# Performance work log

Hardware: AMD Instinct MI355X
Metric: run time of the kernel (lower is better)

## Reference

```python
import jax, jax.numpy as jnp
import numpy as np

DIM = 1024; HEADS = 16; HEAD = 64; FFN_H = 4096
LE = 8; TOPK = 2; DIM_E = 512; DIM_S = 1024
B = 1; S = 2048; N = B * S; NMOE = 2
THETA = 10000.0; EPS = 1e-6; RSF = 1.0


def rmsnorm(x, g):
    return x * jax.lax.rsqrt(jnp.mean(x * x, axis=-1, keepdims=True) + EPS) * g


def rotary(x):
    # x: [b, h, s, a]; matches RotaryEmb: split halves, y1=x1*cos+x2*sin, y2=-x1*sin+x2*cos
    a = x.shape[-1]; s = x.shape[2]
    inv_freq = (1.0 / THETA) ** (jnp.arange(0, a, 2, dtype=jnp.float32) / a)
    freqs = jnp.arange(s, dtype=jnp.float32)[:, None] * inv_freq[None, :]  # [s, a/2]
    cos, sin = jnp.cos(freqs), jnp.sin(freqs)
    x1, x2 = jnp.split(x, 2, axis=-1)
    return jnp.concatenate([x1 * cos + x2 * sin, -x1 * sin + x2 * cos], axis=-1)


def attention(x, attn_w, attn_o, doc):
    # causal + same-document masked attention (flex_attention mask_mod equivalent)
    b, s, d = x.shape
    xq, xk, xv = jnp.split(x @ attn_w, 3, axis=-1)
    def heads(t):
        return t.reshape(b, s, HEADS, HEAD).transpose(0, 2, 1, 3)
    xq, xk, xv = heads(xq), heads(xk), heads(xv)
    xq, xk = rotary(xq), rotary(xk)
    scores = jnp.einsum('bhqa,bhka->bhqk', xq, xk) / jnp.sqrt(jnp.float32(HEAD))
    q_idx = jnp.arange(s)
    mask = (q_idx[:, None] >= q_idx[None, :])[None] & (doc[:, :, None] == doc[:, None, :])
    scores = jnp.where(mask[:, None, :, :], scores, -jnp.inf)
    probs = jax.nn.softmax(scores, axis=-1)
    out = jnp.einsum('bhqk,bhka->bhqa', probs, xv)
    return out.transpose(0, 2, 1, 3).reshape(b, s, d) @ attn_o


def dense_layer(x, aw, ao, up, down, ag, fg, doc):
    xi = attention(rmsnorm(x, ag), aw, ao, doc) + x
    xf = rmsnorm(xi, fg)
    x1, x2 = jnp.split(xf @ up, 2, axis=-1)
    return (jax.nn.silu(x1) * x2) @ down + xi


def moe_layer(x, aw, ao, ag, fg, experts, tkeys, rbias, sup, sdown, idx, vals, doc):
    xi = attention(rmsnorm(x, ag), aw, ao, doc) + x
    xf = rmsnorm(xi, fg)                     # [b,s,d]
    flat = xf.reshape(-1, DIM)               # [N,d]
    # routing: base values + token-key logits + bias, sigmoid, renormalize
    tv = flat @ tkeys                        # [N,le]
    vals = vals + jnp.take_along_axis(tv, idx, axis=-1) + rbias[idx]
    sc = jax.nn.sigmoid(vals)
    sc = sc / jnp.sum(sc, axis=-1, keepdims=True) * RSF   # [N,k]
    # grouped-gemm experts (SwiGLU per expert); dense-over-experts then gather
    h1 = jnp.einsum('nd,edh->neh', flat, experts[0])
    h2 = jnp.einsum('nd,edh->neh', flat, experts[1])
    y_all = jnp.einsum('neh,edh->ned', jax.nn.silu(h1) * h2, experts[2])
    y_sel = jnp.take_along_axis(y_all, idx[:, :, None], axis=1)   # [N,k,d]
    y = jnp.sum(y_sel * sc[:, :, None], axis=1).reshape(xf.shape)
    # shared expert
    x1, x2 = jnp.split(xf @ sup, 2, axis=-1)
    y = y + (jax.nn.silu(x1) * x2) @ sdown
    return y + xi


def setup_inputs() -> dict:
    key = jax.random.key(0)
    ks = jax.random.split(key, 24)
    w = lambda k, shp: (jax.random.normal(k, shp, dtype=jnp.float32) * 0.02)
    inp = {
        'x': jax.random.normal(ks[0], (B, S, DIM), dtype=jnp.float32),
        'doc': jnp.sort(jax.random.randint(ks[1], (B, S), 0, 4), axis=-1).astype(jnp.int32),
        'indices': jax.random.randint(ks[2], (NMOE, N, TOPK), 0, LE).astype(jnp.int64),
        'values': jax.random.normal(ks[3], (NMOE, N, TOPK), dtype=jnp.float32),
        # 2 dense layers (first_k=1, last_k=1)
        'dense_attn_w': w(ks[4], (2, DIM, 3 * DIM)),
        'dense_attn_o': w(ks[5], (2, DIM, DIM)),
        'dense_ffn_up': w(ks[6], (2, DIM, 2 * FFN_H)),
        'dense_ffn_down': w(ks[7], (2, FFN_H, DIM)),
        'dense_attn_g': jnp.ones((2, DIM), dtype=jnp.float32),
        'dense_ffn_g': jnp.ones((2, DIM), dtype=jnp.float32),
        # 2 MoE layers
        'moe_attn_w': w(ks[8], (NMOE, DIM, 3 * DIM)),
        'moe_attn_o': w(ks[9], (NMOE, DIM, DIM)),
        'moe_attn_g': jnp.ones((NMOE, DIM), dtype=jnp.float32),
        'moe_ffn_g': jnp.ones((NMOE, DIM), dtype=jnp.float32),
        'moe_experts': w(ks[10], (NMOE, 3, LE, DIM, DIM_E)),
        'moe_token_keys': w(ks[11], (NMOE, DIM, LE)),
        'moe_router_bias': jnp.zeros((NMOE, LE), dtype=jnp.float32),
        'moe_shared_up': w(ks[12], (NMOE, DIM, 2 * DIM_S)),
        'moe_shared_down': w(ks[13], (NMOE, DIM_S, DIM)),
    }
    return inp


def reference(x, doc, indices, values, dense_attn_w, dense_attn_o, dense_ffn_up,
              dense_ffn_down, dense_attn_g, dense_ffn_g, moe_attn_w, moe_attn_o,
              moe_attn_g, moe_ffn_g, moe_experts, moe_token_keys, moe_router_bias,
              moe_shared_up, moe_shared_down):
    x = dense_layer(x, dense_attn_w[0], dense_attn_o[0], dense_ffn_up[0],
                    dense_ffn_down[0], dense_attn_g[0], dense_ffn_g[0], doc)
    for i in range(NMOE):
        x = moe_layer(x, moe_attn_w[i], moe_attn_o[i], moe_attn_g[i], moe_ffn_g[i],
                      moe_experts[i], moe_token_keys[i], moe_router_bias[i],
                      moe_shared_up[i], moe_shared_down[i], indices[i], values[i], doc)
    x = dense_layer(x, dense_attn_w[1], dense_attn_o[1], dense_ffn_up[1],
                    dense_ffn_down[1], dense_attn_g[1], dense_ffn_g[1], doc)
    return x
```

## Files before the change

### kernel.cpp

```cpp
#include <hip/hip_runtime.h>
#include <cmath>
#include <cstddef>
#include <cstdint>

#define DIMM   1024
#define HEADS  16
#define HEADD  64
#define FFN_H  4096
#define LE     8
#define TOPK   2
#define DIM_E  512
#define DIM_S  1024
#define NTOK   2048

typedef __bf16 bf16x8 __attribute__((ext_vector_type(8)));
typedef float  f32x4  __attribute__((ext_vector_type(4)));

union BF4 { __bf16 h[4]; uint2 u; };
union BF2 { __bf16 h[2]; uint32_t u; };

__device__ __forceinline__ void ldg_lds16(const __bf16* g, __bf16* l) {
    __builtin_amdgcn_global_load_lds(
        (const __attribute__((address_space(1))) uint32_t*)g,
        (__attribute__((address_space(3))) uint32_t*)l, 16, 0, 0);
}

__global__ __launch_bounds__(256) void rmsnorm_bf(
    const float* __restrict__ x, const float* __restrict__ g,
    __bf16* __restrict__ y)
{
    const int row = blockIdx.x;
    const int t = threadIdx.x;
    const float* xr = x + (size_t)row * DIMM;
    float4 v = *(const float4*)(xr + t * 4);
    float ss = v.x * v.x + v.y * v.y + v.z * v.z + v.w * v.w;
    #pragma unroll
    for (int off = 32; off > 0; off >>= 1) ss += __shfl_down(ss, off, 64);
    __shared__ float ws[4];
    if ((t & 63) == 0) ws[t >> 6] = ss;
    __syncthreads();
    const float tot = ws[0] + ws[1] + ws[2] + ws[3];
    const float scale = rsqrtf(tot * (1.0f / DIMM) + 1e-6f);
    const float4 gv = *(const float4*)(g + t * 4);
    BF4 o;
    o.h[0] = (__bf16)(v.x * scale * gv.x);
    o.h[1] = (__bf16)(v.y * scale * gv.y);
    o.h[2] = (__bf16)(v.z * scale * gv.z);
    o.h[3] = (__bf16)(v.w * scale * gv.w);
    *(uint2*)(y + (size_t)row * DIMM + t * 4) = o.u;
}

template <typename OutT>
__global__ __launch_bounds__(256) void gemm_bf_t(
    const __bf16* __restrict__ A, const __bf16* __restrict__ BT,
    const float* __restrict__ add, OutT* __restrict__ C,
    int M, int N, int K)
{
    __shared__ __bf16 As[128 * 32];
    __shared__ __bf16 Bs[128 * 32];
    const int t = threadIdx.x;
    const int m0 = blockIdx.y * 128, n0 = blockIdx.x * 128;
    const int lane = t & 63;
    const int wv = t >> 6;
    const int mw = (wv >> 1) * 64, nw = (wv & 1) * 64;
    const int fr = lane & 15;
    const int fk = ((lane >> 4) ^ ((fr >> 1) & 3)) * 8;
    const int r0 = t >> 2;
    const int q0l = (t & 3) * 8;
    const int q0s = ((t & 3) ^ ((t >> 3) & 3)) * 8;

    const __bf16* gA0 = A + (size_t)(m0 + r0) * K + q0s;
    const __bf16* gA1 = A + (size_t)(m0 + 64 + r0) * K + q0s;
    const __bf16* gB0 = BT + (size_t)(n0 + r0) * K + q0s;
    const __bf16* gB1 = BT + (size_t)(n0 + 64 + r0) * K + q0s;
    __bf16* lA0 = &As[r0 * 32 + q0l];
    __bf16* lA1 = &As[(64 + r0) * 32 + q0l];
    __bf16* lB0 = &Bs[r0 * 32 + q0l];
    __bf16* lB1 = &Bs[(64 + r0) * 32 + q0l];

    f32x4 acc[4][4];
    #pragma unroll
    for (int i = 0; i < 4; ++i)
        #pragma unroll
        for (int j = 0; j < 4; ++j) acc[i][j] = (f32x4){0.f, 0.f, 0.f, 0.f};

    for (int k0 = 0; k0 < K; k0 += 32) {
        __syncthreads();
        ldg_lds16(gA0 + k0, lA0);
        ldg_lds16(gA1 + k0, lA1);
        ldg_lds16(gB0 + k0, lB0);
        ldg_lds16(gB1 + k0, lB1);
        __syncthreads();
        bf16x8 af[4], bfr[4];
        #pragma unroll
        for (int i = 0; i < 4; ++i) {
            af[i]  = *(const bf16x8*)&As[(mw + i * 16 + fr) * 32 + fk];
            bfr[i] = *(const bf16x8*)&Bs[(nw + i * 16 + fr) * 32 + fk];
        }
        #pragma unroll
        for (int i = 0; i < 4; ++i)
            #pragma unroll
            for (int j = 0; j < 4; ++j)
                acc[i][j] = __builtin_amdgcn_mfma_f32_16x16x32_bf16(
                    af[i], bfr[j], acc[i][j], 0, 0, 0);
    }
    const int cn = lane & 15, cr = (lane >> 4) * 4;
    #pragma unroll
    for (int i = 0; i < 4; ++i)
        #pragma unroll
        for (int j = 0; j < 4; ++j)
            #pragma unroll
            for (int r = 0; r < 4; ++r) {
                const size_t off = (size_t)(m0 + mw + i * 16 + cr + r) * N
                                 + (n0 + nw + j * 16 + cn);
                if constexpr (__is_same(OutT, float))
                    C[off] = acc[i][j][r] + (add ? add[off] : 0.f);
                else
                    C[off] = (__bf16)acc[i][j][r];
            }
}

__global__ __launch_bounds__(256) void gemm_qkv_rot(
    const __bf16* __restrict__ A, const __bf16* __restrict__ BT,
    __bf16* __restrict__ C, int M, int N, int K)
{
    __shared__ __bf16 As[128 * 32];
    __shared__ __bf16 Bs[128 * 32];
    const int t = threadIdx.x;
    const int m0 = blockIdx.y * 128, n0 = blockIdx.x * 128;
    const int lane = t & 63;
    const int wv = t >> 6;
    const int mw = (wv >> 1) * 64, nw = (wv & 1) * 64;
    const int fr = lane & 15;
    const int fk = ((lane >> 4) ^ ((fr >> 1) & 3)) * 8;
// ... 129 lines not shown
    const int cn = lane & 15, cr = (lane >> 4) * 4;
    #pragma unroll
    for (int i = 0; i < 4; ++i)
        #pragma unroll
        for (int j = 0; j < 4; ++j)
            #pragma unroll
            for (int r = 0; r < 4; ++r) {
                const size_t off = (size_t)(m0 + mw + i * 16 + cr + r) * N
                                 + (n0 + nw + j * 16 + cn);
                Pz[off] = acc[i][j][r];
            }
}

__global__ __launch_bounds__(256) void gemm_glu(
    const __bf16* __restrict__ A, const __bf16* __restrict__ BT,
    const float* __restrict__ sc, __bf16* __restrict__ G,
    int M, int Nout, int K, int pairOff)
{
    __shared__ __bf16 As[128 * 32];
    __shared__ __bf16 Bs[128 * 32];
    const int t = threadIdx.x;
    const int m0 = blockIdx.y * 128;
    const int b  = blockIdx.x;
    const int lane = t & 63;
    const int wv = t >> 6;
    const int mw = (wv >> 1) * 64, nw = (wv & 1) * 64;
    const int fr = lane & 15;
    const int fk = ((lane >> 4) ^ ((fr >> 1) & 3)) * 8;
    const int r0 = t >> 2;
    const int q0l = (t & 3) * 8;
    const int q0s = ((t & 3) ^ ((t >> 3) & 3)) * 8;

    const int grow0 = b * 64 + ((r0 >> 6) ? 32 : 0) + (r0 & 31)
                    + ((r0 >> 5) & 1) * pairOff;
    const int grow1 = grow0 + 32;

    const __bf16* gA0 = A + (size_t)(m0 + r0) * K + q0s;
    const __bf16* gA1 = A + (size_t)(m0 + 64 + r0) * K + q0s;
    const __bf16* gB0 = BT + (size_t)grow0 * K + q0s;
    const __bf16* gB1 = BT + (size_t)grow1 * K + q0s;
    __bf16* lA0 = &As[r0 * 32 + q0l];
    __bf16* lA1 = &As[(64 + r0) * 32 + q0l];
    __bf16* lB0 = &Bs[r0 * 32 + q0l];
    __bf16* lB1 = &Bs[(64 + r0) * 32 + q0l];

    f32x4 acc[4][4];
    #pragma unroll
    for (int i = 0; i < 4; ++i)
        #pragma unroll
// ... 8 lines not shown
        __syncthreads();
        bf16x8 af[4], bfr[4];
        #pragma unroll
        for (int i = 0; i < 4; ++i) {
            af[i]  = *(const bf16x8*)&As[(mw + i * 16 + fr) * 32 + fk];
            bfr[i] = *(const bf16x8*)&Bs[(nw + i * 16 + fr) * 32 + fk];
        }
        #pragma unroll
        for (int i = 0; i < 4; ++i)
            #pragma unroll
            for (int j = 0; j < 4; ++j)
                acc[i][j] = __builtin_amdgcn_mfma_f32_16x16x32_bf16(
                    af[i], bfr[j], acc[i][j], 0, 0, 0);
    }
    const int cn = lane & 15, cr = (lane >> 4) * 4;
    const int e = (b * 64) >> 9;
    #pragma unroll
    for (int i = 0; i < 4; ++i)
        #pragma unroll
        for (int r = 0; r < 4; ++r) {
            const int m = m0 + mw + i * 16 + cr + r;
            const float s = sc ? sc[m * LE + e] : 1.f;
            #pragma unroll
            for (int j = 0; j < 2; ++j) {
                const float h1 = acc[i][j][r];
                const float h2 = acc[i][j + 2][r];
                const float o = (h1 / (1.f + __expf(-h1))) * h2 * s;
                const int col = b * 64 + (nw >> 1) + j * 16 + cn;
                G[(size_t)m * Nout + col] = (__bf16)o;
            }
        }
}

__global__ __launch_bounds__(512, 2) void gemm_glu256(
    const __bf16* __restrict__ A, const __bf16* __restrict__ BT,
    const float* __restrict__ sc, __bf16* __restrict__ G,
    int M, int Nout, int K, int pairOff)
{
    __shared__ __bf16 As[4][256 * 32];
    __shared__ __bf16 Bs[4][256 * 32];
    const int t = threadIdx.x;
    const int m0 = blockIdx.y * 256;
    const int b  = blockIdx.x;
    const int lane = t & 63;
    const int wv = t >> 6;
    const int wr = wv >> 2, wc = wv & 3;
    const int fr = lane & 15;
    const int fk = ((lane >> 4) ^ ((fr >> 1) & 3)) * 8;

    const int r0 = t >> 2;
    const int c  = t & 3;
    const int cs = (c ^ ((r0 >> 1) & 3)) * 8;
    const int ldst = r0 * 32 + c * 8;

    const int rem0 = r0 & 63;
    const int grow0 = b * 128 + (r0 >> 6) * 32 + ((rem0 >> 4) & 1) * 16
                    + (rem0 & 15) + (rem0 >> 5) * pairOff;
    const int r1 = r0 + 128;
    const int rem1 = r1 & 63;
    const int grow1 = b * 128 + (r1 >> 6) * 32 + ((rem1 >> 4) & 1) * 16
                    + (rem1 & 15) + (rem1 >> 5) * pairOff;

    const __bf16* gA0 = A + (size_t)(m0 + r0) * K + cs;
    const __bf16* gA1 = A + (size_t)(m0 + 128 + r0) * K + cs;
    const __bf16* gB0 = BT + (size_t)grow0 * K + cs;
    const __bf16* gB1 = BT + (size_t)grow1 * K + cs;

    const int NT = K >> 5;

#define STAGE256(bi, kt) do {                                   \
        const int _k = (kt) << 5;                               \
        ldg_lds16(gA0 + _k, &As[bi][ldst]);                     \
        ldg_lds16(gA1 + _k, &As[bi][128 * 32 + ldst]);          \
        ldg_lds16(gB0 + _k, &Bs[bi][ldst]);                     \
        ldg_lds16(gB1 + _k, &Bs[bi][128 * 32 + ldst]);          \
    } while (0)

    f32x4 acc[8][4];
    #pragma unroll
    for (int i = 0; i < 8; ++i)
        #pragma unroll
        for (int j = 0; j < 4; ++j) acc[i][j] = (f32x4){0.f, 0.f, 0.f, 0.f};

    STAGE256(0, 0);
    STAGE256(1, 1);
    STAGE256(2, 2);
    asm volatile("s_waitcnt vmcnt(8)" ::: "memory");
    __builtin_amdgcn_s_barrier();
    asm volatile("" ::: "memory");

    for (int kt = 0; kt < NT; ++kt) {
        const int bi = kt & 3;
        if (kt + 3 < NT) STAGE256((kt + 3) & 3, kt + 3);

        bf16x8 af[8], bf[4];
        const __bf16* Ab = &As[bi][(wr * 128 + fr) * 32 + fk];
        #pragma unroll
        for (int i = 0; i < 8; ++i) af[i] = *(const bf16x8*)(Ab + i * 16 * 32);
        const __bf16* Bb = &Bs[bi][(wc * 64 + fr) * 32 + fk];
        #pragma unroll
        for (int j = 0; j < 4; ++j) bf[j] = *(const bf16x8*)(Bb + j * 16 * 32);

        #pragma unroll
        for (int i = 0; i < 8; ++i)
            #pragma unroll
            for (int j = 0; j < 4; ++j)
                acc[i][j] = __builtin_amdgcn_mfma_f32_16x16x32_bf16(
                    af[i], bf[j], acc[i][j], 0, 0, 0);

        if (kt < NT - 1) {
            if (kt < NT - 3)       asm volatile("s_waitcnt vmcnt(8)" ::: "memory");
            else if (kt == NT - 3) asm volatile("s_waitcnt vmcnt(4)" ::: "memory");
            else                   asm volatile("s_waitcnt vmcnt(0)" ::: "memory");
            __builtin_amdgcn_s_barrier();
            asm volatile("" ::: "memory");
        }
    }
#undef STAGE256

    const int cn = lane & 15, cr = (lane >> 4) * 4;
    const int e = b >> 2;
    #pragma unroll
    for (int i = 0; i < 8; ++i)
        #pragma unroll
        for (int r = 0; r < 4; ++r) {
            const int m = m0 + wr * 128 + i * 16 + cr + r;
            const float s = sc ? sc[m * LE + e] : 1.f;
            #pragma unroll
            for (int j = 0; j < 2; ++j) {
                const float h1 = acc[i][j][r];
                const float h2 = acc[i][j + 2][r];
                const float o = (h1 / (1.f + __expf(-h1))) * h2 * s;
                const int col = b * 128 + wc * 32 + j * 16 + cn;
                G[(size_t)m * Nout + col] = (__bf16)o;
            }
        }
}

__global__ __launch_bounds__(256) void reduce4_add(
    const float* __restrict__ P, const float* __restrict__ add,
    float* __restrict__ out, size_t MN)
{
    const size_t i = ((size_t)blockIdx.x * 256 + threadIdx.x) * 4;
    float4 s  = *(const float4*)(P + i);
    const float4 s1 = *(const float4*)(P + MN + i);
    const float4 s2 = *(const float4*)(P + 2 * MN + i);
    const float4 s3 = *(const float4*)(P + 3 * MN + i);
    const float4 a  = *(const float4*)(add + i);
    s.x += s1.x + s2.x + s3.x + a.x;
    s.y += s1.y + s2.y + s3.y + a.y;
    s.z += s1.z + s2.z + s3.z + a.z;
    s.w += s1.w + s2.w + s3.w + a.w;
    *(float4*)(out + i) = s;
}

__global__ __launch_bounds__(256) void reduce2_add(
    const float* __restrict__ P, const float* __restrict__ add,
    float* __restrict__ out, size_t MN)
{
    const size_t i = ((size_t)blockIdx.x * 256 + threadIdx.x) * 4;
    float4 s  = *(const float4*)(P + i);
    const float4 s1 = *(const float4*)(P + MN + i);
    const float4 a  = *(const float4*)(add + i);
    s.x += s1.x + a.x;
    s.y += s1.y + a.y;
    s.z += s1.z + a.z;
    s.w += s1.w + a.w;
    *(float4*)(out + i) = s;
}

__global__ __launch_bounds__(256) void transpose_cast(
    const float* __restrict__ in, __bf16* __restrict__ out, int R, int C)
{
    __shared__ float tile[32][33];
    const int bx = blockIdx.x * 32, by = blockIdx.y * 32;
    const size_t bz = (size_t)blockIdx.z * R * C;
    const int tx = threadIdx.x & 31, ty = threadIdx.x >> 5;
    const float* ip = in + bz;
    __bf16* op = out + bz;
    #pragma unroll
    for (int i = 0; i < 4; ++i)
        tile[ty + i * 8][tx] = ip[(size_t)(by + ty + i * 8) * C + bx + tx];
    __syncthreads();
// ... 150 lines not shown
                oacc[nb] = __builtin_amdgcn_mfma_f32_16x16x32_bf16(pf, vf, oacc[nb], 0, 0, 0);
            }
        }
    }
    float inv[4];
    #pragma unroll
    for (int rg = 0; rg < 4; ++rg) inv[rg] = 1.f / lrow[rg];
    #pragma unroll
    for (int nb = 0; nb < 4; ++nb)
        #pragma unroll
        for (int rg = 0; rg < 4; ++rg)
            out[(size_t)(q0w + lhi * 4 + rg) * DIMM + h * 64 + nb * 16 + l15] =
                (__bf16)(oacc[nb][rg] * inv[rg]);
}

__global__ __launch_bounds__(64) void router_bf(
    const __bf16* __restrict__ xf, const float* __restrict__ tkeys,
    const float* __restrict__ rbias, const int* __restrict__ idx,
    const float* __restrict__ vals, float* __restrict__ sc)
{
    const int n = blockIdx.x;
    const int t = threadIdx.x;
    const int e0 = idx[n * 2 + 0], e1 = idx[n * 2 + 1];
    float a0 = 0.f, a1 = 0.f;
    for (int d = t; d < DIMM; d += 64) {
        const float xv = (float)xf[(size_t)n * DIMM + d];
        a0 += xv * tkeys[d * LE + e0];
        a1 += xv * tkeys[d * LE + e1];
    }
    #pragma unroll
    for (int off = 32; off > 0; off >>= 1) {
        a0 += __shfl_down(a0, off, 64);
        a1 += __shfl_down(a1, off, 64);
    }
    if (t == 0) {
        const float v0 = vals[n * 2 + 0] + a0 + rbias[e0];
        const float v1 = vals[n * 2 + 1] + a1 + rbias[e1];
        const float s0 = 1.f / (1.f + __expf(-v0));
        const float s1 = 1.f / (1.f + __expf(-v1));
        const float inv = 1.f / (s0 + s1);
        float r[LE];
        #pragma unroll
        for (int e = 0; e < LE; ++e) r[e] = 0.f;
        r[e0] += s0 * inv;
        r[e1] += s1 * inv;
        #pragma unroll
        for (int e = 0; e < LE; ++e) sc[n * LE + e] = r[e];
    }
}

struct Scratch {
    float *qkv, *xi, *t1, *sc, *xA, *xB, *part;
    __bf16 *qkvb, *xn_bf, *attnO_bf, *xf_bf, *wbuf, *gact_bf, *gs_bf;
};

static void attn_block(const float* x_in, const __bf16* awT, const __bf16* aoT,
                       const float* ag, const int* doc, Scratch& w, hipStream_t s)
{
    rmsnorm_bf<<<NTOK, 256, 0, s>>>(x_in, ag, w.xn_bf);
    gemm_qkv_rot<<<dim3(24, 16), 256, 0, s>>>(w.xn_bf, awT, w.qkvb, NTOK, 3072, 1024);
    attn_mfma<<<dim3(HEADS, NTOK / 64), 256, 0, s>>>(w.qkvb, doc, w.attnO_bf);
    gemm_bf_splitk<<<dim3(8, 16, 2), 256, 0, s>>>(w.attnO_bf, aoT, w.qkv, NTOK, 1024, 1024, 512);
    reduce2_add<<<(NTOK * 1024) / 1024, 256, 0, s>>>(w.qkv, x_in, w.xi, (size_t)NTOK * 1024);
}

static void dense_layer_run(const float* x_in, float* x_out,
                            const float* aw, const float* ao,
                            const float* up, const float* down,
                            const float* ag, const float* fg,
                            const int* doc, Scratch& w, hipStream_t s)
{
    __bf16* awT = w.wbuf;
    __bf16* aoT = w.wbuf + 3145728;
    __bf16* upT = w.wbuf + 4194304;
    __bf16* dnT = w.wbuf + 12582912;
    transpose_cast<<<dim3(96, 32, 1), 256, 0, s>>>(aw, awT, 1024, 3072);
    transpose_cast<<<dim3(32, 32, 1), 256, 0, s>>>(ao, aoT, 1024, 1024);
    transpose_cast<<<dim3(256, 32, 1), 256, 0, s>>>(up, upT, 1024, 8192);
    transpose_cast<<<dim3(32, 128, 1), 256, 0, s>>>(down, dnT, 4096, 1024);
    attn_block(x_in, awT, aoT, ag, doc, w, s);
    rmsnorm_bf<<<NTOK, 256, 0, s>>>(w.xi, fg, w.xf_bf);
    gemm_glu256<<<dim3(32, 8), 512, 0, s>>>(w.xf_bf, upT, nullptr, w.gact_bf, NTOK, 4096, 1024, 4096);
    gemm_bf_splitk<<<dim3(8, 16, 4), 256, 0, s>>>(w.gact_bf, dnT, w.part, NTOK, 1024, 4096, 1024);
    reduce4_add<<<(NTOK * 1024) / 1024, 256, 0, s>>>(w.part, w.xi, x_out, (size_t)NTOK * 1024);
}

static void moe_layer_run(const float* x_in, float* x_out,
                          const float* aw, const float* ao,
                          const float* ag, const float* fg,
                          const float* experts, const float* tkeys,
                          const float* rbias, const float* sup,
                          const float* sdn, const int* idx, const float* vals,
                          const int* doc, Scratch& w, hipStream_t s)
{
    __bf16* awT  = w.wbuf;
    __bf16* aoT  = w.wbuf + 3145728;
    __bf16* w01T = w.wbuf + 4194304;
    __bf16* w2c  = w.wbuf + 12582912;
    __bf16* supT = w.wbuf + 16777216;
    __bf16* sdnT = w.wbuf + 18874368;
    const size_t EW = (size_t)LE * DIMM * DIM_E;
    transpose_cast<<<dim3(96, 32, 1), 256, 0, s>>>(aw, awT, 1024, 3072);
    transpose_cast<<<dim3(32, 32, 1), 256, 0, s>>>(ao, aoT, 1024, 1024);
    transpose_cast<<<dim3(16, 32, 8), 256, 0, s>>>(experts, w01T, 1024, 512);
    transpose_cast<<<dim3(16, 32, 8), 256, 0, s>>>(experts + EW, w01T + 4194304, 1024, 512);
    cast_w2<<<16384, 256, 0, s>>>(experts + 2 * EW, w2c);
    transpose_cast<<<dim3(64, 32, 1), 256, 0, s>>>(sup, supT, 1024, 2048);
    transpose_cast<<<dim3(32, 32, 1), 256, 0, s>>>(sdn, sdnT, 1024, 1024);

    attn_block(x_in, awT, aoT, ag, doc, w, s);
    rmsnorm_bf<<<NTOK, 256, 0, s>>>(w.xi, fg, w.xf_bf);
    router_bf<<<NTOK, 64, 0, s>>>(w.xf_bf, tkeys, rbias, idx, vals, w.sc);
    gemm_glu256<<<dim3(32, 8), 512, 0, s>>>(w.xf_bf, w01T, w.sc, w.gact_bf, NTOK, 4096, 1024, 4096);
    gemm_glu<<<dim3(16, 16), 256, 0, s>>>(w.xf_bf, supT, nullptr, w.gs_bf, NTOK, 1024, 1024, 1024);
    gemm_bf_splitk<<<dim3(8, 16, 2), 256, 0, s>>>(w.gs_bf, sdnT, w.part, NTOK, 1024, 1024, 512);
    reduce2_add<<<(NTOK * 1024) / 1024, 256, 0, s>>>(w.part, w.xi, w.t1, (size_t)NTOK * 1024);
    gemm_bf_splitk<<<dim3(8, 16, 4), 256, 0, s>>>(w.gact_bf, w2c, w.part, NTOK, 1024, 4096, 1024);
    reduce4_add<<<(NTOK * 1024) / 1024, 256, 0, s>>>(w.part, w.t1, x_out, (size_t)NTOK * 1024);
}

extern "C" void kernel_launch(void* const* d_in, const int* in_sizes, int n_in,
                              void* d_out, int out_size, void* d_ws, size_t ws_size,
                              hipStream_t stream)
{
    (void)in_sizes; (void)n_in; (void)out_size; (void)ws_size;
    const float* x       = (const float*)d_in[0];
    const int*   doc     = (const int*)d_in[1];
    const int*   indices = (const int*)d_in[2];
    const float* values  = (const float*)d_in[3];
    const float* d_aw    = (const float*)d_in[4];
    const float* d_ao    = (const float*)d_in[5];
    const float* d_up    = (const float*)d_in[6];
    const float* d_down  = (const float*)d_in[7];
// ... 3 lines not shown
    const float* m_ao    = (const float*)d_in[11];
    const float* m_ag    = (const float*)d_in[12];
    const float* m_fg    = (const float*)d_in[13];
    const float* m_ex    = (const float*)d_in[14];
    const float* m_tk    = (const float*)d_in[15];
    const float* m_rb    = (const float*)d_in[16];
    const float* m_sup   = (const float*)d_in[17];
    const float* m_sdn   = (const float*)d_in[18];

    Scratch w;
    float* f = (float*)d_ws;
    w.qkv = f; f += 6291456;
    w.xi  = f; f += 2097152;
    float* h12 = f; f += 16777216;
    w.t1  = h12 + 8388608;
    w.sc  = f; f += 16384;
    w.xA  = f; f += 2097152;
    w.xB  = f; f += 2097152;
    __bf16* b = (__bf16*)f;
    w.xn_bf    = b; b += 2097152;
    w.attnO_bf = b; b += 2097152;
    w.xf_bf    = b; b += 2097152;
    w.wbuf     = b; b += 19922944;
    w.qkvb     = (__bf16*)w.qkv;
    w.gact_bf  = (__bf16*)w.qkv;
    w.gs_bf    = (__bf16*)w.qkv + 8388608;
    w.part     = h12;

    float* out = (float*)d_out;

    dense_layer_run(x, w.xA, d_aw, d_ao, d_up, d_down, d_ag, d_fg, doc, w, stream);
    const size_t EXL = (size_t)3 * LE * DIMM * DIM_E;
    moe_layer_run(w.xA, w.xB,
                  m_aw, m_ao, m_ag, m_fg,
                  m_ex, m_tk, m_rb, m_sup, m_sdn,
                  indices, values, doc, w, stream);
    moe_layer_run(w.xB, w.xA,
                  m_aw + (size_t)DIMM * 3 * DIMM, m_ao + (size_t)DIMM * DIMM,
                  m_ag + DIMM, m_fg + DIMM,
                  m_ex + EXL, m_tk + DIMM * LE, m_rb + LE,
                  m_sup + (size_t)DIMM * 2 * DIM_S, m_sdn + (size_t)DIM_S * DIMM,
                  indices + (size_t)NTOK * TOPK, values + (size_t)NTOK * TOPK,
                  doc, w, stream);
    dense_layer_run(w.xA, out,
                    d_aw + (size_t)DIMM * 3 * DIMM, d_ao + (size_t)DIMM * DIMM,
                    d_up + (size_t)DIMM * 2 * FFN_H, d_down + (size_t)FFN_H * DIMM,
                    d_ag + DIMM, d_fg + DIMM, doc, w, stream);
}
```

Baseline: 1.242 ms.

## Replace dense all-expert MoE with token-scattered sparse expert GEMMs; fuse rmsnorm into reductions

Before this change, every token ran through all 8 experts and the routing scores were applied as per-expert multipliers, most of them zero. Now a router_scatter kernel builds per-expert token lists of capacity 1024. Grouped GEMMs (gemm_glu_moe, gemm_moe_down) compute only the routed top-2 pairs, and a gather kernel combines the results with the residual. Separately, the rmsnorm launches are folded into the split-K reduce kernels so the next layer's normalized bf16 input comes out of the reduction. The costs are atomics-based scatter, gathered A rows and a hard capacity limit per expert.

```diff
diff --git a/kernel.cpp b/kernel.cpp
--- a/kernel.cpp
+++ b/kernel.cpp
@@ -12,6 +12,7 @@
 #define DIM_E  512
 #define DIM_S  1024
 #define NTOK   2048
+#define CAP    1024
 
 typedef __bf16 bf16x8 __attribute__((ext_vector_type(8)));
 typedef float  f32x4  __attribute__((ext_vector_type(4)));
@@ -25,99 +26,35 @@
         (__attribute__((address_space(3))) uint32_t*)l, 16, 0, 0);
 }
 
-__global__ __launch_bounds__(256) void rmsnorm_bf(
-    const float* __restrict__ x, const float* __restrict__ g,
-    __bf16* __restrict__ y)
-{
-    const int row = blockIdx.x;
-    const int t = threadIdx.x;
-    const float* xr = x + (size_t)row * DIMM;
-    float4 v = *(const float4*)(xr + t * 4);
-    float ss = v.x * v.x + v.y * v.y + v.z * v.z + v.w * v.w;
+__device__ __forceinline__ void row_norm_write(
+    float4 s, const float* __restrict__ g, __bf16* __restrict__ yn,
+    int row, int t)
+{
+    __shared__ float ws[4];
+    float ss = s.x * s.x + s.y * s.y + s.z * s.z + s.w * s.w;
     #pragma unroll
     for (int off = 32; off > 0; off >>= 1) ss += __shfl_down(ss, off, 64);
-    __shared__ float ws[4];
     if ((t & 63) == 0) ws[t >> 6] = ss;
     __syncthreads();
     const float tot = ws[0] + ws[1] + ws[2] + ws[3];
     const float scale = rsqrtf(tot * (1.0f / DIMM) + 1e-6f);
     const float4 gv = *(const float4*)(g + t * 4);
     BF4 o;
-    o.h[0] = (__bf16)(v.x * scale * gv.x);
-    o.h[1] = (__bf16)(v.y * scale * gv.y);
-    o.h[2] = (__bf16)(v.z * scale * gv.z);
-    o.h[3] = (__bf16)(v.w * scale * gv.w);
-    *(uint2*)(y + (size_t)row * DIMM + t * 4) = o.u;
-}
-
-template <typename OutT>
-__global__ __launch_bounds__(256) void gemm_bf_t(
-    const __bf16* __restrict__ A, const __bf16* __restrict__ BT,
-    const float* __restrict__ add, OutT* __restrict__ C,
-    int M, int N, int K)
-{
-    __shared__ __bf16 As[128 * 32];
-    __shared__ __bf16 Bs[128 * 32];
-    const int t = threadIdx.x;
-    const int m0 = blockIdx.y * 128, n0 = blockIdx.x * 128;
-    const int lane = t & 63;
-    const int wv = t >> 6;
-    const int mw = (wv >> 1) * 64, nw = (wv & 1) * 64;
-    const int fr = lane & 15;
-    const int fk = ((lane >> 4) ^ ((fr >> 1) & 3)) * 8;
-    const int r0 = t >> 2;
-    const int q0l = (t & 3) * 8;
-    const int q0s = ((t & 3) ^ ((t >> 3) & 3)) * 8;
-
-    const __bf16* gA0 = A + (size_t)(m0 + r0) * K + q0s;
-    const __bf16* gA1 = A + (size_t)(m0 + 64 + r0) * K + q0s;
-    const __bf16* gB0 = BT + (size_t)(n0 + r0) * K + q0s;
-    const __bf16* gB1 = BT + (size_t)(n0 + 64 + r0) * K + q0s;
-    __bf16* lA0 = &As[r0 * 32 + q0l];
-    __bf16* lA1 = &As[(64 + r0) * 32 + q0l];
-    __bf16* lB0 = &Bs[r0 * 32 + q0l];
-    __bf16* lB1 = &Bs[(64 + r0) * 32 + q0l];
-
-    f32x4 acc[4][4];
-    #pragma unroll
-    for (int i = 0; i < 4; ++i)
-        #pragma unroll
-        for (int j = 0; j < 4; ++j) acc[i][j] = (f32x4){0.f, 0.f, 0.f, 0.f};
-
-    for (int k0 = 0; k0 < K; k0 += 32) {
-        __syncthreads();
-        ldg_lds16(gA0 + k0, lA0);
-        ldg_lds16(gA1 + k0, lA1);
-        ldg_lds16(gB0 + k0, lB0);
-        ldg_lds16(gB1 + k0, lB1);
-        __syncthreads();
-        bf16x8 af[4], bfr[4];
-        #pragma unroll
-        for (int i = 0; i < 4; ++i) {
-            af[i]  = *(const bf16x8*)&As[(mw + i * 16 + fr) * 32 + fk];
-            bfr[i] = *(const bf16x8*)&Bs[(nw + i * 16 + fr) * 32 + fk];
-        }
-        #pragma unroll
-        for (int i = 0; i < 4; ++i)
-            #pragma unroll
-            for (int j = 0; j < 4; ++j)
-                acc[i][j] = __builtin_amdgcn_mfma_f32_16x16x32_bf16(
-                    af[i], bfr[j], acc[i][j], 0, 0, 0);
-    }
-    const int cn = lane & 15, cr = (lane >> 4) * 4;
-    #pragma unroll
-    for (int i = 0; i < 4; ++i)
-        #pragma unroll
-        for (int j = 0; j < 4; ++j)
-            #pragma unroll
-            for (int r = 0; r < 4; ++r) {
-                const size_t off = (size_t)(m0 + mw + i * 16 + cr + r) * N
-                                 + (n0 + nw + j * 16 + cn);
-                if constexpr (__is_same(OutT, float))
-                    C[off] = acc[i][j][r] + (add ? add[off] : 0.f);
-                else
-                    C[off] = (__bf16)acc[i][j][r];
-            }
+    o.h[0] = (__bf16)(s.x * scale * gv.x);
+    o.h[1] = (__bf16)(s.y * scale * gv.y);
+    o.h[2] = (__bf16)(s.z * scale * gv.z);
+    o.h[3] = (__bf16)(s.w * scale * gv.w);
+    *(uint2*)(yn + (size_t)row * DIMM + t * 4) = o.u;
+}
+
+__global__ __launch_bounds__(256) void rmsnorm_bf(
+    const float* __restrict__ x, const float* __restrict__ g,
+    __bf16* __restrict__ y)
+{
+    const int row = blockIdx.x;
+    const int t = threadIdx.x;
+    float4 v = *(const float4*)(x + (size_t)row * DIMM + t * 4);
+    row_norm_write(v, g, y, row, t);
 }
 
 __global__ __launch_bounds__(256) void gemm_qkv_rot(
@@ -277,8 +214,7 @@
 
 __global__ __launch_bounds__(256) void gemm_glu(
     const __bf16* __restrict__ A, const __bf16* __restrict__ BT,
-    const float* __restrict__ sc, __bf16* __restrict__ G,
-    int M, int Nout, int K, int pairOff)
+    __bf16* __restrict__ G, int M, int Nout, int K, int pairOff)
 {
     __shared__ __bf16 As[128 * 32];
     __shared__ __bf16 Bs[128 * 32];
@@ -294,8 +230,7 @@
     const int q0l = (t & 3) * 8;
     const int q0s = ((t & 3) ^ ((t >> 3) & 3)) * 8;
 
-    const int grow0 = b * 64 + ((r0 >> 6) ? 32 : 0) + (r0 & 31)
-                    + ((r0 >> 5) & 1) * pairOff;
+    const int grow0 = b * 64 + (r0 & 31) + ((r0 >> 5) & 1) * pairOff;
     const int grow1 = grow0 + 32;
 
     const __bf16* gA0 = A + (size_t)(m0 + r0) * K + q0s;
@@ -334,134 +269,181 @@
                     af[i], bfr[j], acc[i][j], 0, 0, 0);
     }
     const int cn = lane & 15, cr = (lane >> 4) * 4;
-    const int e = (b * 64) >> 9;
     #pragma unroll
     for (int i = 0; i < 4; ++i)
         #pragma unroll
         for (int r = 0; r < 4; ++r) {
             const int m = m0 + mw + i * 16 + cr + r;
-            const float s = sc ? sc[m * LE + e] : 1.f;
+            #pragma unroll
+            for (int j = 0; j < 2; ++j) {
+                const float h1 = acc[i][j][r];
+                const float h2 = acc[i][j + 2][r];
+                const float o = (h1 / (1.f + __expf(-h1))) * h2;
+                const int col = b * 64 + (nw >> 1) + j * 16 + cn;
+                G[(size_t)m * Nout + col] = (__bf16)o;
+            }
+        }
+}
+
+__global__ __launch_bounds__(256) void gemm_glu_moe(
+    const __bf16* __restrict__ A, const __bf16* __restrict__ BT,
+    const int* __restrict__ cnt, const int* __restrict__ tok,
+    const float* __restrict__ ssc, __bf16* __restrict__ H)
+{
+    __shared__ __bf16 As[128 * 32];
+    __shared__ __bf16 Bs[128 * 32];
+    const int e = blockIdx.z;
+    const int ce = cnt[e];
+    const int m0 = blockIdx.y * 128;
+    if (m0 >= ce) return;
+    const int b = blockIdx.x;
+    const int t = threadIdx.x;
+    const int lane = t & 63;
+    const int wv = t >> 6;
+    const int mw = (wv >> 1) * 64, nw = (wv & 1) * 64;
+    const int fr = lane & 15;
+    const int fk = ((lane >> 4) ^ ((fr >> 1) & 3)) * 8;
+    const int r0 = t >> 2;
+    const int q0l = (t & 3) * 8;
+    const int q0s = ((t & 3) ^ ((t >> 3) & 3)) * 8;
+    const int base = e * CAP;
+
+    int ri0 = m0 + r0;      if (ri0 > ce - 1) ri0 = ce - 1;
+    int ri1 = m0 + 64 + r0; if (ri1 > ce - 1) ri1 = ce - 1;
+    const int tid0 = tok[base + ri0];
+    const int tid1 = tok[base + ri1];
+    const int grow0 = e * 512 + b * 64 + (r0 & 31) + ((r0 >> 5) & 1) * 4096;
+    const int grow1 = grow0 + 32;
+
+    const __bf16* gA0 = A + (size_t)tid0 * 1024 + q0s;
+    const __bf16* gA1 = A + (size_t)tid1 * 1024 + q0s;
+    const __bf16* gB0 = BT + (size_t)grow0 * 1024 + q0s;
+    const __bf16* gB1 = BT + (size_t)grow1 * 1024 + q0s;
+    __bf16* lA0 = &As[r0 * 32 + q0l];
+    __bf16* lA1 = &As[(64 + r0) * 32 + q0l];
+    __bf16* lB0 = &Bs[r0 * 32 + q0l];
+    __bf16* lB1 = &Bs[(64 + r0) * 32 + q0l];
+
+    f32x4 acc[4][4];
+    #pragma unroll
+    for (int i = 0; i < 4; ++i)
+        #pragma unroll
+        for (int j = 0; j < 4; ++j) acc[i][j] = (f32x4){0.f, 0.f, 0.f, 0.f};
+
+    for (int k0 = 0; k0 < 1024; k0 += 32) {
+        __syncthreads();
+        ldg_lds16(gA0 + k0, lA0);
+        ldg_lds16(gA1 + k0, lA1);
+        ldg_lds16(gB0 + k0, lB0);
+        ldg_lds16(gB1 + k0, lB1);
+        __syncthreads();
+        bf16x8 af[4], bfr[4];
+        #pragma unroll
+        for (int i = 0; i < 4; ++i) {
+            af[i]  = *(const bf16x8*)&As[(mw + i * 16 + fr) * 32 + fk];
+            bfr[i] = *(const bf16x8*)&Bs[(nw + i * 16 + fr) * 32 + fk];
+        }
+        #pragma unroll
+        for (int i = 0; i < 4; ++i)
+            #pragma unroll
+            for (int j = 0; j < 4; ++j)
+                acc[i][j] = __builtin_amdgcn_mfma_f32_16x16x32_bf16(
+                    af[i], bfr[j], acc[i][j], 0, 0, 0);
+    }
+    const int cn = lane & 15, cr = (lane >> 4) * 4;
+    #pragma unroll
+    for (int i = 0; i < 4; ++i)
+        #pragma unroll
+        for (int r = 0; r < 4; ++r) {
+            const int mr = mw + i * 16 + cr + r;
+            const float s = ssc[base + m0 + mr];
             #pragma unroll
             for (int j = 0; j < 2; ++j) {
                 const float h1 = acc[i][j][r];
                 const float h2 = acc[i][j + 2][r];
                 const float o = (h1 / (1.f + __expf(-h1))) * h2 * s;
                 const int col = b * 64 + (nw >> 1) + j * 16 + cn;
-                G[(size_t)m * Nout + col] = (__bf16)o;
-            }
-        }
-}
-
-__global__ __launch_bounds__(512, 2) void gemm_glu256(
-    const __bf16* __restrict__ A, const __bf16* __restrict__ BT,
-    const float* __restrict__ sc, __bf16* __restrict__ G,
-    int M, int Nout, int K, int pairOff)
-{
-    __shared__ __bf16 As[4][256 * 32];
-    __shared__ __bf16 Bs[4][256 * 32];
-    const int t = threadIdx.x;
-    const int m0 = blockIdx.y * 256;
-    const int b  = blockIdx.x;
+                H[(size_t)(base + m0 + mr) * 512 + col] = (__bf16)o;
+            }
+        }
+}
+
+__global__ __launch_bounds__(256) void gemm_moe_down(
+    const __bf16* __restrict__ H, const __bf16* __restrict__ W2,
+    const int* __restrict__ cnt, float* __restrict__ Y)
+{
+    __shared__ __bf16 As[128 * 32];
+    __shared__ __bf16 Bs[128 * 32];
+    const int e = blockIdx.z;
+    const int ce = cnt[e];
+    const int m0 = blockIdx.y * 128;
+    if (m0 >= ce) return;
+    const int n0 = blockIdx.x * 128;
+    const int t = threadIdx.x;
     const int lane = t & 63;
     const int wv = t >> 6;
-    const int wr = wv >> 2, wc = wv & 3;
+    const int mw = (wv >> 1) * 64, nw = (wv & 1) * 64;
     const int fr = lane & 15;
     const int fk = ((lane >> 4) ^ ((fr >> 1) & 3)) * 8;
-
     const int r0 = t >> 2;
-    const int c  = t & 3;
-    const int cs = (c ^ ((r0 >> 1) & 3)) * 8;
-    const int ldst = r0 * 32 + c * 8;
-
-    const int rem0 = r0 & 63;
-    const int grow0 = b * 128 + (r0 >> 6) * 32 + ((rem0 >> 4) & 1) * 16
-                    + (rem0 & 15) + (rem0 >> 5) * pairOff;
-    const int r1 = r0 + 128;
-    const int rem1 = r1 & 63;
-    const int grow1 = b * 128 + (r1 >> 6) * 32 + ((rem1 >> 4) & 1) * 16
-                    + (rem1 & 15) + (rem1 >> 5) * pairOff;
-
-    const __bf16* gA0 = A + (size_t)(m0 + r0) * K + cs;
-    const __bf16* gA1 = A + (size_t)(m0 + 128 + r0) * K + cs;
-    const __bf16* gB0 = BT + (size_t)grow0 * K + cs;
-    const __bf16* gB1 = BT + (size_t)grow1 * K + cs;
-
-    const int NT = K >> 5;
-
-#define STAGE256(bi, kt) do {                                   \
-        const int _k = (kt) << 5;                               \
-        ldg_lds16(gA0 + _k, &As[bi][ldst]);                     \
-        ldg_lds16(gA1 + _k, &As[bi][128 * 32 + ldst]);          \
-        ldg_lds16(gB0 + _k, &Bs[bi][ldst]);                     \
-        ldg_lds16(gB1 + _k, &Bs[bi][128 * 32 + ldst]);          \
-    } while (0)
-
-    f32x4 acc[8][4];
-    #pragma unroll
-    for (int i = 0; i < 8; ++i)
+    const int q0l = (t & 3) * 8;
+    const int q0s = ((t & 3) ^ ((t >> 3) & 3)) * 8;
+    const int base = e * CAP;
+
+    const __bf16* gA0 = H + (size_t)(base + m0 + r0) * 512 + q0s;
+    const __bf16* gA1 = H + (size_t)(base + m0 + 64 + r0) * 512 + q0s;
+    const __bf16* gB0 = W2 + (size_t)(n0 + r0) * 4096 + e * 512 + q0s;
+    const __bf16* gB1 = W2 + (size_t)(n0 + 64 + r0) * 4096 + e * 512 + q0s;
+    __bf16* lA0 = &As[r0 * 32 + q0l];
+    __bf16* lA1 = &As[(64 + r0) * 32 + q0l];
+    __bf16* lB0 = &Bs[r0 * 32 + q0l];
+    __bf16* lB1 = &Bs[(64 + r0) * 32 + q0l];
+
+    f32x4 acc[4][4];
+    #pragma unroll
+    for (int i = 0; i < 4; ++i)
         #pragma unroll
         for (int j = 0; j < 4; ++j) acc[i][j] = (f32x4){0.f, 0.f, 0.f, 0.f};
 
-    STAGE256(0, 0);
-    STAGE256(1, 1);
-    STAGE256(2, 2);
-    asm volatile("s_waitcnt vmcnt(8)" ::: "memory");
-    __builtin_amdgcn_s_barrier();
-    asm volatile("" ::: "memory");
-
-    for (int kt = 0; kt < NT; ++kt) {
-        const int bi = kt & 3;
-        if (kt + 3 < NT) STAGE256((kt + 3) & 3, kt + 3);
-
-        bf16x8 af[8], bf[4];
-        const __bf16* Ab = &As[bi][(wr * 128 + fr) * 32 + fk];
-        #pragma unroll
-        for (int i = 0; i < 8; ++i) af[i] = *(const bf16x8*)(Ab + i * 16 * 32);
-        const __bf16* Bb = &Bs[bi][(wc * 64 + fr) * 32 + fk];
-        #pragma unroll
-        for (int j = 0; j < 4; ++j) bf[j] = *(const bf16x8*)(Bb + j * 16 * 32);
-
-        #pragma unroll
-        for (int i = 0; i < 8; ++i)
+    for (int k0 = 0; k0 < 512; k0 += 32) {
+        __syncthreads();
+        ldg_lds16(gA0 + k0, lA0);
+        ldg_lds16(gA1 + k0, lA1);
+        ldg_lds16(gB0 + k0, lB0);
+        ldg_lds16(gB1 + k0, lB1);
+        __syncthreads();
+        bf16x8 af[4], bfr[4];
+        #pragma unroll
+        for (int i = 0; i < 4; ++i) {
+            af[i]  = *(const bf16x8*)&As[(mw + i * 16 + fr) * 32 + fk];
+            bfr[i] = *(const bf16x8*)&Bs[(nw + i * 16 + fr) * 32 + fk];
+        }
+        #pragma unroll
+        for (int i = 0; i < 4; ++i)
             #pragma unroll
             for (int j = 0; j < 4; ++j)
                 acc[i][j] = __builtin_amdgcn_mfma_f32_16x16x32_bf16(
-                    af[i], bf[j], acc[i][j], 0, 0, 0);
-
-        if (kt < NT - 1) {
-            if (kt < NT - 3)       asm volatile("s_waitcnt vmcnt(8)" ::: "memory");
-            else if (kt == NT - 3) asm volatile("s_waitcnt vmcnt(4)" ::: "memory");
-            else                   asm volatile("s_waitcnt vmcnt(0)" ::: "memory");
-            __builtin_amdgcn_s_barrier();
-            asm volatile("" ::: "memory");
-        }
-    }
-#undef STAGE256
-
+                    af[i], bfr[j], acc[i][j], 0, 0, 0);
+    }
     const int cn = lane & 15, cr = (lane >> 4) * 4;
-    const int e = b >> 2;
-    #pragma unroll
-    for (int i = 0; i < 8; ++i)
-        #pragma unroll
-        for (int r = 0; r < 4; ++r) {
-            const int m = m0 + wr * 128 + i * 16 + cr + r;
-            const float s = sc ? sc[m * LE + e] : 1.f;
-            #pragma unroll
-            for (int j = 0; j < 2; ++j) {
-                const float h1 = acc[i][j][r];
-                const float h2 = acc[i][j + 2][r];
-                const float o = (h1 / (1.f + __expf(-h1))) * h2 * s;
-                const int col = b * 128 + wc * 32 + j * 16 + cn;
-                G[(size_t)m * Nout + col] = (__bf16)o;
-            }
-        }
-}
-
-__global__ __launch_bounds__(256) void reduce4_add(
+    #pragma unroll
+    for (int i = 0; i < 4; ++i)
+        #pragma unroll
+        for (int j = 0; j < 4; ++j)
+            #pragma unroll
+            for (int r = 0; r < 4; ++r)
+                Y[(size_t)(base + m0 + mw + i * 16 + cr + r) * 1024
+                  + (n0 + nw + j * 16 + cn)] = acc[i][j][r];
+}
+
+__global__ __launch_bounds__(256) void reduce4_norm(
     const float* __restrict__ P, const float* __restrict__ add,
-    float* __restrict__ out, size_t MN)
-{
-    const size_t i = ((size_t)blockIdx.x * 256 + threadIdx.x) * 4;
+    float* __restrict__ out, const float* __restrict__ g,
+    __bf16* __restrict__ yn, size_t MN)
+{
+    const int row = blockIdx.x;
+    const int t = threadIdx.x;
+    const size_t i = (size_t)row * 1024 + t * 4;
     float4 s  = *(const float4*)(P + i);
     const float4 s1 = *(const float4*)(P + MN + i);
     const float4 s2 = *(const float4*)(P + 2 * MN + i);
@@ -472,13 +454,17 @@
     s.z += s1.z + s2.z + s3.z + a.z;
     s.w += s1.w + s2.w + s3.w + a.w;
     *(float4*)(out + i) = s;
-}
-
-__global__ __launch_bounds__(256) void reduce2_add(
+    if (g) row_norm_write(s, g, yn, row, t);
+}
+
+__global__ __launch_bounds__(256) void reduce2_norm(
     const float* __restrict__ P, const float* __restrict__ add,
-    float* __restrict__ out, size_t MN)
-{
-    const size_t i = ((size_t)blockIdx.x * 256 + threadIdx.x) * 4;
+    float* __restrict__ out, const float* __restrict__ g,
+    __bf16* __restrict__ yn, size_t MN)
+{
+    const int row = blockIdx.x;
+    const int t = threadIdx.x;
+    const size_t i = (size_t)row * 1024 + t * 4;
     float4 s  = *(const float4*)(P + i);
     const float4 s1 = *(const float4*)(P + MN + i);
     const float4 a  = *(const float4*)(add + i);
@@ -487,6 +473,29 @@
     s.z += s1.z + a.z;
     s.w += s1.w + a.w;
     *(float4*)(out + i) = s;
+    if (g) row_norm_write(s, g, yn, row, t);
+}
+
+__global__ __launch_bounds__(256) void moe_gather_norm(
+    const float* __restrict__ Y, const int* __restrict__ slots,
+    const float* __restrict__ t1, float* __restrict__ out,
+    const float* __restrict__ g, __bf16* __restrict__ yn)
+{
+    const int n = blockIdx.x;
+    const int t = threadIdx.x;
+    const int s0 = slots[n * 2 + 0];
+    const int s1 = slots[n * 2 + 1];
+    const size_t i = (size_t)n * 1024 + t * 4;
+    const float4 a = *(const float4*)(Y + (size_t)s0 * 1024 + t * 4);
+    const float4 b = *(const float4*)(Y + (size_t)s1 * 1024 + t * 4);
+    const float4 c = *(const float4*)(t1 + i);
+    float4 s;
+    s.x = a.x + b.x + c.x;
+    s.y = a.y + b.y + c.y;
+    s.z = a.z + b.z + c.z;
+    s.w = a.w + b.w + c.w;
+    *(float4*)(out + i) = s;
+    if (g) row_norm_write(s, g, yn, n, t);
 }
 
 __global__ __launch_bounds__(256) void transpose_cast(
@@ -667,10 +676,16 @@
                 (__bf16)(oacc[nb][rg] * inv[rg]);
 }
 
-__global__ __launch_bounds__(64) void router_bf(
+__global__ __launch_bounds__(64) void zero_cnt(int* __restrict__ cnt)
+{
+    if (threadIdx.x < LE) cnt[threadIdx.x] = 0;
+}
+
+__global__ __launch_bounds__(64) void router_scatter(
     const __bf16* __restrict__ xf, const float* __restrict__ tkeys,
     const float* __restrict__ rbias, const int* __restrict__ idx,
-    const float* __restrict__ vals, float* __restrict__ sc)
+    const float* __restrict__ vals, int* __restrict__ cnt,
+    int* __restrict__ tok, float* __restrict__ ssc, int* __restrict__ slots)
 {
     const int n = blockIdx.x;
     const int t = threadIdx.x;
@@ -692,35 +707,141 @@
         const float s0 = 1.f / (1.f + __expf(-v0));
         const float s1 = 1.f / (1.f + __expf(-v1));
         const float inv = 1.f / (s0 + s1);
-        float r[LE];
-        #pragma unroll
-        for (int e = 0; e < LE; ++e) r[e] = 0.f;
-        r[e0] += s0 * inv;
-        r[e1] += s1 * inv;
-        #pragma unroll
-        for (int e = 0; e < LE; ++e) sc[n * LE + e] = r[e];
-    }
+        int p0 = atomicAdd(&cnt[e0], 1);
+        if (p0 > CAP - 1) p0 = CAP - 1;
+        tok[e0 * CAP + p0] = n;
+        ssc[e0 * CAP + p0] = s0 * inv;
+        slots[n * 2 + 0] = e0 * CAP + p0;
+        int p1 = atomicAdd(&cnt[e1], 1);
+        if (p1 > CAP - 1) p1 = CAP - 1;
+        tok[e1 * CAP + p1] = n;
+        ssc[e1 * CAP + p1] = s1 * inv;
+        slots[n * 2 + 1] = e1 * CAP + p1;
+    }
+}
+
+__global__ __launch_bounds__(512, 2) void gemm_glu256(
+    const __bf16* __restrict__ A, const __bf16* __restrict__ BT,
+    __bf16* __restrict__ G, int M, int Nout, int K, int pairOff)
+{
+    __shared__ __bf16 As[4][256 * 32];
+    __shared__ __bf16 Bs[4][256 * 32];
+    const int t = threadIdx.x;
+    const int m0 = blockIdx.y * 256;
+    const int b  = blockIdx.x;
+    const int lane = t & 63;
+    const int wv = t >> 6;
+    const int wr = wv >> 2, wc = wv & 3;
+    const int fr = lane & 15;
+    const int fk = ((lane >> 4) ^ ((fr >> 1) & 3)) * 8;
+
+    const int r0 = t >> 2;
+    const int c  = t & 3;
+    const int cs = (c ^ ((r0 >> 1) & 3)) * 8;
+    const int ldst = r0 * 32 + c * 8;
+
+    const int rem0 = r0 & 63;
+    const int grow0 = b * 128 + (r0 >> 6) * 32 + ((rem0 >> 4) & 1) * 16
+                    + (rem0 & 15) + (rem0 >> 5) * pairOff;
+    const int r1 = r0 + 128;
+    const int rem1 = r1 & 63;
+    const int grow1 = b * 128 + (r1 >> 6) * 32 + ((rem1 >> 4) & 1) * 16
+                    + (rem1 & 15) + (rem1 >> 5) * pairOff;
+
+    const __bf16* gA0 = A + (size_t)(m0 + r0) * K + cs;
+    const __bf16* gA1 = A + (size_t)(m0 + 128 + r0) * K + cs;
+    const __bf16* gB0 = BT + (size_t)grow0 * K + cs;
+    const __bf16* gB1 = BT + (size_t)grow1 * K + cs;
+
+    const int NT = K >> 5;
+
+#define STAGE256(bi, kt) do {                                   \
+        const int _k = (kt) << 5;                               \
+        ldg_lds16(gA0 + _k, &As[bi][ldst]);                     \
+        ldg_lds16(gA1 + _k, &As[bi][128 * 32 + ldst]);          \
+        ldg_lds16(gB0 + _k, &Bs[bi][ldst]);                     \
+        ldg_lds16(gB1 + _k, &Bs[bi][128 * 32 + ldst]);          \
+    } while (0)
+
+    f32x4 acc[8][4];
+    #pragma unroll
+    for (int i = 0; i < 8; ++i)
+        #pragma unroll
+        for (int j = 0; j < 4; ++j) acc[i][j] = (f32x4){0.f, 0.f, 0.f, 0.f};
+
+    STAGE256(0, 0);
+    STAGE256(1, 1);
+    STAGE256(2, 2);
+    asm volatile("s_waitcnt vmcnt(8)" ::: "memory");
+    __builtin_amdgcn_s_barrier();
+    asm volatile("" ::: "memory");
+
+    for (int kt = 0; kt < NT; ++kt) {
+        const int bi = kt & 3;
+        if (kt + 3 < NT) STAGE256((kt + 3) & 3, kt + 3);
+
+        bf16x8 af[8], bf[4];
+        const __bf16* Ab = &As[bi][(wr * 128 + fr) * 32 + fk];
+        #pragma unroll
+        for (int i = 0; i < 8; ++i) af[i] = *(const bf16x8*)(Ab + i * 16 * 32);
+        const __bf16* Bb = &Bs[bi][(wc * 64 + fr) * 32 + fk];
+        #pragma unroll
+        for (int j = 0; j < 4; ++j) bf[j] = *(const bf16x8*)(Bb + j * 16 * 32);
+
+        #pragma unroll
+        for (int i = 0; i < 8; ++i)
+            #pragma unroll
+            for (int j = 0; j < 4; ++j)
+                acc[i][j] = __builtin_amdgcn_mfma_f32_16x16x32_bf16(
+                    af[i], bf[j], acc[i][j], 0, 0, 0);
+
+        if (kt < NT - 1) {
+            if (kt < NT - 3)       asm volatile("s_waitcnt vmcnt(8)" ::: "memory");
+            else if (kt == NT - 3) asm volatile("s_waitcnt vmcnt(4)" ::: "memory");
+            else                   asm volatile("s_waitcnt vmcnt(0)" ::: "memory");
+            __builtin_amdgcn_s_barrier();
+            asm volatile("" ::: "memory");
+        }
+    }
+#undef STAGE256
+
+    const int cn = lane & 15, cr = (lane >> 4) * 4;
+    #pragma unroll
+    for (int i = 0; i < 8; ++i)
+        #pragma unroll
+        for (int r = 0; r < 4; ++r) {
+            const int m = m0 + wr * 128 + i * 16 + cr + r;
+            #pragma unroll
+            for (int j = 0; j < 2; ++j) {
+                const float h1 = acc[i][j][r];
+                const float h2 = acc[i][j + 2][r];
+                const float o = (h1 / (1.f + __expf(-h1))) * h2;
+                const int col = b * 128 + wc * 32 + j * 16 + cn;
+                G[(size_t)m * Nout + col] = (__bf16)o;
+            }
+        }
 }
 
 struct Scratch {
-    float *qkv, *xi, *t1, *sc, *xA, *xB, *part;
-    __bf16 *qkvb, *xn_bf, *attnO_bf, *xf_bf, *wbuf, *gact_bf, *gs_bf;
+    float *qkv, *xi, *t1, *yslot, *xA, *xB, *part, *slot_sc;
+    int *cnt, *tok, *slots;
+    __bf16 *qkvb, *xn_bf, *attnO_bf, *xf_bf, *wbuf, *gact_bf, *gs_bf, *hbuf;
 };
 
-static void attn_block(const float* x_in, const __bf16* awT, const __bf16* aoT,
-                       const float* ag, const int* doc, Scratch& w, hipStream_t s)
-{
-    rmsnorm_bf<<<NTOK, 256, 0, s>>>(x_in, ag, w.xn_bf);
-    gemm_qkv_rot<<<dim3(24, 16), 256, 0, s>>>(w.xn_bf, awT, w.qkvb, NTOK, 3072, 1024);
+static void attn_block(const float* x_in, const __bf16* xn,
+                       const __bf16* awT, const __bf16* aoT,
+                       const float* fg, const int* doc, Scratch& w, hipStream_t s)
+{
+    gemm_qkv_rot<<<dim3(24, 16), 256, 0, s>>>(xn, awT, w.qkvb, NTOK, 3072, 1024);
     attn_mfma<<<dim3(HEADS, NTOK / 64), 256, 0, s>>>(w.qkvb, doc, w.attnO_bf);
     gemm_bf_splitk<<<dim3(8, 16, 2), 256, 0, s>>>(w.attnO_bf, aoT, w.qkv, NTOK, 1024, 1024, 512);
-    reduce2_add<<<(NTOK * 1024) / 1024, 256, 0, s>>>(w.qkv, x_in, w.xi, (size_t)NTOK * 1024);
+    reduce2_norm<<<NTOK, 256, 0, s>>>(w.qkv, x_in, w.xi, fg, w.xf_bf, (size_t)NTOK * 1024);
 }
 
 static void dense_layer_run(const float* x_in, float* x_out,
                             const float* aw, const float* ao,
                             const float* up, const float* down,
-                            const float* ag, const float* fg,
+                            const float* fg, const float* g_next,
                             const int* doc, Scratch& w, hipStream_t s)
 {
     __bf16* awT = w.wbuf;
@@ -731,16 +852,15 @@
     transpose_cast<<<dim3(32, 32, 1), 256, 0, s>>>(ao, aoT, 1024, 1024);
     transpose_cast<<<dim3(256, 32, 1), 256, 0, s>>>(up, upT, 1024, 8192);
     transpose_cast<<<dim3(32, 128, 1), 256, 0, s>>>(down, dnT, 4096, 1024);
-    attn_block(x_in, awT, aoT, ag, doc, w, s);
-    rmsnorm_bf<<<NTOK, 256, 0, s>>>(w.xi, fg, w.xf_bf);
-    gemm_glu256<<<dim3(32, 8), 512, 0, s>>>(w.xf_bf, upT, nullptr, w.gact_bf, NTOK, 4096, 1024, 4096);
+    attn_block(x_in, w.xn_bf, awT, aoT, fg, doc, w, s);
+    gemm_glu256<<<dim3(32, 8), 512, 0, s>>>(w.xf_bf, upT, w.gact_bf, NTOK, 4096, 1024, 4096);
     gemm_bf_splitk<<<dim3(8, 16, 4), 256, 0, s>>>(w.gact_bf, dnT, w.part, NTOK, 1024, 4096, 1024);
-    reduce4_add<<<(NTOK * 1024) / 1024, 256, 0, s>>>(w.part, w.xi, x_out, (size_t)NTOK * 1024);
+    reduce4_norm<<<NTOK, 256, 0, s>>>(w.part, w.xi, x_out, g_next, w.xn_bf, (size_t)NTOK * 1024);
 }
 
 static void moe_layer_run(const float* x_in, float* x_out,
                           const float* aw, const float* ao,
-                          const float* ag, const float* fg,
+                          const float* fg, const float* g_next,
                           const float* experts, const float* tkeys,
                           const float* rbias, const float* sup,
                           const float* sdn, const int* idx, const float* vals,
@@ -761,15 +881,17 @@
     transpose_cast<<<dim3(64, 32, 1), 256, 0, s>>>(sup, supT, 1024, 2048);
     transpose_cast<<<dim3(32, 32, 1), 256, 0, s>>>(sdn, sdnT, 1024, 1024);
 
-    attn_block(x_in, awT, aoT, ag, doc, w, s);
-    rmsnorm_bf<<<NTOK, 256, 0, s>>>(w.xi, fg, w.xf_bf);
-    router_bf<<<NTOK, 64, 0, s>>>(w.xf_bf, tkeys, rbias, idx, vals, w.sc);
-    gemm_glu256<<<dim3(32, 8), 512, 0, s>>>(w.xf_bf, w01T, w.sc, w.gact_bf, NTOK, 4096, 1024, 4096);
-    gemm_glu<<<dim3(16, 16), 256, 0, s>>>(w.xf_bf, supT, nullptr, w.gs_bf, NTOK, 1024, 1024, 1024);
+    attn_block(x_in, w.xn_bf, awT, aoT, fg, doc, w, s);
+    zero_cnt<<<1, 64, 0, s>>>(w.cnt);
+    router_scatter<<<NTOK, 64, 0, s>>>(w.xf_bf, tkeys, rbias, idx, vals,
+                                       w.cnt, w.tok, w.slot_sc, w.slots);
+    gemm_glu_moe<<<dim3(8, CAP / 128, LE), 256, 0, s>>>(
+        w.xf_bf, w01T, w.cnt, w.tok, w.slot_sc, w.hbuf);
+    gemm_glu<<<dim3(16, 16), 256, 0, s>>>(w.xf_bf, supT, w.gs_bf, NTOK, 1024, 1024, 1024);
     gemm_bf_splitk<<<dim3(8, 16, 2), 256, 0, s>>>(w.gs_bf, sdnT, w.part, NTOK, 1024, 1024, 512);
-    reduce2_add<<<(NTOK * 1024) / 1024, 256, 0, s>>>(w.part, w.xi, w.t1, (size_t)NTOK * 1024);
-    gemm_bf_splitk<<<dim3(8, 16, 4), 256, 0, s>>>(w.gact_bf, w2c, w.part, NTOK, 1024, 4096, 1024);
-    reduce4_add<<<(NTOK * 1024) / 1024, 256, 0, s>>>(w.part, w.t1, x_out, (size_t)NTOK * 1024);
+    reduce2_norm<<<NTOK, 256, 0, s>>>(w.part, w.xi, w.t1, nullptr, nullptr, (size_t)NTOK * 1024);
+    gemm_moe_down<<<dim3(8, CAP / 128, LE), 256, 0, s>>>(w.hbuf, w2c, w.cnt, w.yslot);
+    moe_gather_norm<<<NTOK, 256, 0, s>>>(w.yslot, w.slots, w.t1, x_out, g_next, w.xn_bf);
 }
 
 extern "C" void kernel_launch(void* const* d_in, const int* in_sizes, int n_in,
@@ -803,9 +925,14 @@
     w.xi  = f; f += 2097152;
     float* h12 = f; f += 16777216;
     w.t1  = h12 + 8388608;
-    w.sc  = f; f += 16384;
     w.xA  = f; f += 2097152;
     w.xB  = f; f += 2097152;
+    int* ip = (int*)f;
+    w.cnt   = ip; ip += 16;
+    w.tok   = ip; ip += LE * CAP;
+    w.slots = ip; ip += NTOK * 2;
+    f = (float*)ip;
+    w.slot_sc = f; f += LE * CAP;
     __bf16* b = (__bf16*)f;
     w.xn_bf    = b; b += 2097152;
     w.attnO_bf = b; b += 2097152;
@@ -813,20 +940,24 @@
     w.wbuf     = b; b += 19922944;
     w.qkvb     = (__bf16*)w.qkv;
     w.gact_bf  = (__bf16*)w.qkv;
+    w.hbuf     = (__bf16*)w.qkv;
     w.gs_bf    = (__bf16*)w.qkv + 8388608;
     w.part     = h12;
+    w.yslot    = h12;
 
     float* out = (float*)d_out;
 
-    dense_layer_run(x, w.xA, d_aw, d_ao, d_up, d_down, d_ag, d_fg, doc, w, stream);
+    rmsnorm_bf<<<NTOK, 256, 0, stream>>>(x, d_ag, w.xn_bf);
+
+    dense_layer_run(x, w.xA, d_aw, d_ao, d_up, d_down, d_fg, m_ag, doc, w, stream);
     const size_t EXL = (size_t)3 * LE * DIMM * DIM_E;
     moe_layer_run(w.xA, w.xB,
-                  m_aw, m_ao, m_ag, m_fg,
+                  m_aw, m_ao, m_fg, m_ag + DIMM,
                   m_ex, m_tk, m_rb, m_sup, m_sdn,
                   indices, values, doc, w, stream);
     moe_layer_run(w.xB, w.xA,
                   m_aw + (size_t)DIMM * 3 * DIMM, m_ao + (size_t)DIMM * DIMM,
-                  m_ag + DIMM, m_fg + DIMM,
+                  m_fg + DIMM, d_ag + DIMM,
                   m_ex + EXL, m_tk + DIMM * LE, m_rb + LE,
                   m_sup + (size_t)DIMM * 2 * DIM_S, m_sdn + (size_t)DIM_S * DIMM,
                   indices + (size_t)NTOK * TOPK, values + (size_t)NTOK * TOPK,
@@ -834,5 +965,5 @@
     dense_layer_run(w.xA, out,
                     d_aw + (size_t)DIMM * 3 * DIMM, d_ao + (size_t)DIMM * DIMM,
                     d_up + (size_t)DIMM * 2 * FFN_H, d_down + (size_t)FFN_H * DIMM,
-                    d_ag + DIMM, d_fg + DIMM, doc, w, stream);
-}
+                    d_fg + DIMM, nullptr, doc, w, stream);
+}
```

Measured after the change: 1.237 ms. Within noise of the previous version (-0.4%).
